# Optimization experiments

Measured on AMD Instinct MI355X. Metric: run time of the kernel, lower is better.

## Reference

```python
import jax, jax.numpy as jnp
import numpy as np

N_NODES = 50000
N_EDGES = 800000
N_GRAPHS = 128
IN_DIM, H1, H2, OUT_DIM = 256, 128, 64, 10


def setup_inputs() -> dict:
    key = jax.random.key(0)
    ks = jax.random.split(key, 8)
    x = jax.random.normal(ks[0], (N_NODES, IN_DIM), dtype=jnp.float32)
    edge_index = jax.random.randint(ks[1], (2, N_EDGES), 0, N_NODES, dtype=jnp.int64 if jax.config.jax_enable_x64 else jnp.int32)
    batch = jnp.sort(jax.random.randint(ks[2], (N_NODES,), 0, N_GRAPHS))
    s1 = 1.0 / np.sqrt(IN_DIM)
    s2 = 1.0 / np.sqrt(H1)
    s3 = 1.0 / np.sqrt(H2)
    W1 = jax.random.uniform(ks[3], (IN_DIM, H1), jnp.float32, -s1, s1)
    b1 = jnp.zeros((H1,), jnp.float32)
    W2 = jax.random.uniform(ks[4], (H1, H2), jnp.float32, -s2, s2)
    b2 = jnp.zeros((H2,), jnp.float32)
    Wfc = jax.random.uniform(ks[5], (H2, OUT_DIM), jnp.float32, -s3, s3)
    bfc = jax.random.uniform(ks[6], (OUT_DIM,), jnp.float32, -s3, s3)
    return {"x": x, "edge_index": edge_index, "batch": batch,
            "W1": W1, "b1": b1, "W2": W2, "b2": b2, "Wfc": Wfc, "bfc": bfc}


def _gcn_norm(edge_index, n_nodes):
    # PyG gcn_norm with add_self_loops=True: D^{-1/2} (A+I) D^{-1/2}
    self_loops = jnp.arange(n_nodes, dtype=edge_index.dtype)
    row = jnp.concatenate([edge_index[0], self_loops])
    col = jnp.concatenate([edge_index[1], self_loops])
    deg = jax.ops.segment_sum(jnp.ones_like(col, dtype=jnp.float32), col,
                              num_segments=n_nodes)
    dis = jnp.where(deg > 0, 1.0 / jnp.sqrt(deg), 0.0)
    norm = dis[row] * dis[col]  # [E + N]
    return row, col, norm


def _gcn_layer(x, W, b, row, col, norm, n_nodes):
    h = x @ W                          # [N, out]
    msg = h[row] * norm[:, None]       # gather + scale: [E+N, out]
    agg = jax.ops.segment_sum(msg, col, num_segments=n_nodes)
    return jax.nn.relu(agg + b)


def reference(x, edge_index, batch, W1, b1, W2, b2, Wfc, bfc):
    n = x.shape[0]
    row, col, norm = _gcn_norm(edge_index, n)
    h = _gcn_layer(x, W1, b1, row, col, norm, n)
    h = _gcn_layer(h, W2, b2, row, col, norm, n)
    # global max pool over graphs
    g = jax.ops.segment_max(h, batch, num_segments=N_GRAPHS)  # [G, H2]
    # dropout is identity at inference
    return g @ Wfc + bfc
```

## Files before the change

### kernel.cpp

```cpp
#include <hip/hip_runtime.h>
#include <math.h>


typedef __attribute__((ext_vector_type(8))) short bfrag;
typedef __attribute__((ext_vector_type(4))) float ffrag;

__device__ inline void bf16split(float f, short& hi, short& lo) {
    unsigned u = __float_as_uint(f);
    unsigned r = u + 0x7fffu + ((u >> 16) & 1u);
    unsigned short h = (unsigned short)(r >> 16);
    float hf = __uint_as_float(((unsigned)h) << 16);
    float lf = f - hf;
    unsigned ul = __float_as_uint(lf);
    unsigned rl = ul + 0x7fffu + ((ul >> 16) & 1u);
    hi = (short)h;
    lo = (short)(rl >> 16);
}

__global__ __launch_bounds__(256) void k_zero(int* __restrict__ cnt, int* __restrict__ pool,
                                              int n1, int n2) {
    int i = blockIdx.x * 256 + threadIdx.x;
    if (i < n1) cnt[i] = 0;
    if (i < n2) pool[i] = 0;
}

__global__ __launch_bounds__(256) void k_count(const int* __restrict__ ei, int* __restrict__ cnt,
                                               int E) {
    int e = blockIdx.x * 256 + threadIdx.x;
    if (e < E) atomicAdd(&cnt[ei[E + e]], 1);
}

__global__ __launch_bounds__(256) void k_dis(const int* __restrict__ cnt, float* __restrict__ dis,
                                             int N) {
    int v = blockIdx.x * 256 + threadIdx.x;
    if (v < N) dis[v] = 1.0f / sqrtf((float)(cnt[v] + 1));
}

__global__ __launch_bounds__(1024) void k_scan_block(const int* __restrict__ cnt,
                                                     int* __restrict__ rowptr,
                                                     int* __restrict__ bsum, int N) {
    __shared__ int lds[1024];
    int t = threadIdx.x;
    int i = blockIdx.x * 1024 + t;
    int val = (i < N) ? cnt[i] : 0;
    lds[t] = val;
    __syncthreads();
    for (int off = 1; off < 1024; off <<= 1) {
        int u = (t >= off) ? lds[t - off] : 0;
        __syncthreads();
        lds[t] += u;
        __syncthreads();
    }
    if (i < N) rowptr[i] = lds[t] - val;
    if (t == 1023) bsum[blockIdx.x] = lds[1023];
}

__global__ __launch_bounds__(1024) void k_scan_tot(const int* __restrict__ bsum,
                                                   int* __restrict__ bsum2, int nb) {
    __shared__ int lds[1024];
    int t = threadIdx.x;
    int val = (t < nb) ? bsum[t] : 0;
    lds[t] = val;
    __syncthreads();
    for (int off = 1; off < 1024; off <<= 1) {
        int u = (t >= off) ? lds[t - off] : 0;
        __syncthreads();
        lds[t] += u;
        __syncthreads();
    }
    if (t < nb) bsum2[t] = lds[t] - val;
}

__global__ __launch_bounds__(256) void k_scan_add(int* __restrict__ rowptr, int* __restrict__ cursor,
                                                  const int* __restrict__ bsum2, int N, int E) {
    int i = blockIdx.x * 256 + threadIdx.x;
    if (i < N) {
        int r = rowptr[i] + bsum2[i >> 10];
        rowptr[i] = r;
        cursor[i] = r;
    }
    if (i == 0) rowptr[N] = E;
}

__global__ __launch_bounds__(256) void k_fill(const int* __restrict__ ei,
                                              const float* __restrict__ dis,
                                              int* __restrict__ cursor,
                                              float2* __restrict__ csr, int E) {
    int e = blockIdx.x * 256 + threadIdx.x;
    if (e >= E) return;
    int r = ei[e];
    int c = ei[E + e];
    int p = atomicAdd(&cursor[c], 1);
    csr[p] = make_float2(__int_as_float(r), dis[r] * dis[c]);
}

__global__ __launch_bounds__(256) void k_wsplit(const float* __restrict__ W,
                                                short* __restrict__ wt_hi,
                                                short* __restrict__ wt_lo) {
    int i = blockIdx.x * 256 + threadIdx.x;
    if (i >= 256 * 128) return;
    int k = i >> 7, c = i & 127;
    short hi, lo;
    bf16split(W[i], hi, lo);
    wt_hi[c * 256 + k] = hi;
    wt_lo[c * 256 + k] = lo;
}

__global__ __launch_bounds__(256) void k_gemm1_mfma(const float* __restrict__ A,
                                                    const short* __restrict__ wt_hi,
                                                    const short* __restrict__ wt_lo,
                                                    float* __restrict__ C, int M) {
    constexpr int KD = 256;
    __shared__ short Ah[64][40];
    __shared__ short Al[64][40];

    const int t = threadIdx.x;
    const int lane = t & 63;
    const int wid = t >> 6;
    const int wr = wid >> 1;
    const int wc = wid & 1;
    const int row0 = blockIdx.x * 64;
    const int lrow = lane & 15;
    const int lkg = lane >> 4;

    ffrag acc[2][4];
#pragma unroll
    for (int mr = 0; mr < 2; mr++)
#pragma unroll
        for (int nr = 0; nr < 4; nr++)
#pragma unroll
            for (int q = 0; q < 4; q++) acc[mr][nr][q] = 0.f;

    for (int kc = 0; kc < KD; kc += 32) {
#pragma unroll
        for (int i = 0; i < 2; i++) {
            int s = t * 2 + i;
            int m = s >> 3;
            int kq = s & 7;
            int r = row0 + m;
            float4 v = make_float4(0.f, 0.f, 0.f, 0.f);
            if (r < M) v = *(const float4*)&A[(size_t)r * KD + kc + kq * 4];
            short4 sh, sl;
            bf16split(v.x, sh.x, sl.x);
            bf16split(v.y, sh.y, sl.y);
            bf16split(v.z, sh.z, sl.z);
            bf16split(v.w, sh.w, sl.w);
            *(short4*)&Ah[m][kq * 4] = sh;
            *(short4*)&Al[m][kq * 4] = sl;
        }
        __syncthreads();

        bfrag ahi[2], alo[2];
#pragma unroll
        for (int mr = 0; mr < 2; mr++) {
            int arow = wr * 32 + mr * 16 + lrow;
            ahi[mr] = *(const bfrag*)&Ah[arow][lkg * 8];
            alo[mr] = *(const bfrag*)&Al[arow][lkg * 8];
        }
#pragma unroll
        for (int nr = 0; nr < 4; nr++) {
            int col = wc * 64 + nr * 16 + lrow;
            const size_t boff = (size_t)col * 256 + kc + lkg * 8;
            bfrag bhi = *(const bfrag*)&wt_hi[boff];
            bfrag blo = *(const bfrag*)&wt_lo[boff];
#pragma unroll
            for (int mr = 0; mr < 2; mr++) {
                acc[mr][nr] = __builtin_amdgcn_mfma_f32_16x16x32_bf16(ahi[mr], bhi, acc[mr][nr], 0, 0, 0);
                acc[mr][nr] = __builtin_amdgcn_mfma_f32_16x16x32_bf16(ahi[mr], blo, acc[mr][nr], 0, 0, 0);
                acc[mr][nr] = __builtin_amdgcn_mfma_f32_16x16x32_bf16(alo[mr], bhi, acc[mr][nr], 0, 0, 0);
            }
        }
        __syncthreads();
    }

#pragma unroll
    for (int mr = 0; mr < 2; mr++)
#pragma unroll
        for (int nr = 0; nr < 4; nr++)
#pragma unroll
            for (int q = 0; q < 4; q++) {
                int rr = row0 + wr * 32 + mr * 16 + lkg * 4 + q;
                int cc = wc * 64 + nr * 16 + lrow;
                if (rr < M) C[(size_t)rr * 128 + cc] = acc[mr][nr][q];
            }
}

template <int KDIM, int NOUT>
__global__ __launch_bounds__(256) void k_gemm(const float* __restrict__ A,
                                              const float* __restrict__ W,
                                              float* __restrict__ C, int M) {
    constexpr int BM = 64, BK = 32;
    constexpr int NGRP = NOUT / 64;
    __shared__ float As[BK][BM + 4];
    __shared__ float Ws[BK][NOUT];

    const int t = threadIdx.x;
    const int tx = t & 15;
    const int ty = t >> 4;
    const int row0 = blockIdx.x * BM;

    float acc[4][4 * NGRP];
#pragma unroll
    for (int r = 0; r < 4; r++)
#pragma unroll
        for (int c = 0; c < 4 * NGRP; c++) acc[r][c] = 0.f;

    for (int kc = 0; kc < KDIM; kc += BK) {
#pragma unroll
        for (int i = 0; i < 2; i++) {
            int s = t * 2 + i;
            int m = s >> 3;
            int kq = s & 7;
            int r = row0 + m;
            float4 v = make_float4(0.f, 0.f, 0.f, 0.f);
            if (r < M) v = *(const float4*)&A[(size_t)r * KDIM + kc + kq * 4];
            As[kq * 4 + 0][m] = v.x;
            As[kq * 4 + 1][m] = v.y;
            As[kq * 4 + 2][m] = v.z;
            As[kq * 4 + 3][m] = v.w;
        }
        constexpr int WLOADS = (BK * NOUT / 4) / 256;
#pragma unroll
        for (int i = 0; i < WLOADS; i++) {
            int s = t + i * 256;
            int k = s / (NOUT / 4);
            int c4 = s % (NOUT / 4);
            *(float4*)&Ws[k][c4 * 4] = *(const float4*)&W[(size_t)(kc + k) * NOUT + c4 * 4];
        }
        __syncthreads();

#pragma unroll
        for (int k = 0; k < BK; k++) {
            float4 a = *(const float4*)&As[k][ty * 4];
            float4 w0 = *(const float4*)&Ws[k][tx * 4];
            float4 w1;
            if (NGRP == 2) w1 = *(const float4*)&Ws[k][64 + tx * 4];
            const float* ap = (const float*)&a;
            const float* w0p = (const float*)&w0;
            const float* w1p = (const float*)&w1;
#pragma unroll
            for (int r = 0; r < 4; r++) {
#pragma unroll
                for (int c = 0; c < 4; c++) {
                    acc[r][c] += ap[r] * w0p[c];
                    if (NGRP == 2) acc[r][4 + c] += ap[r] * w1p[c];
                }
            }
        }
        __syncthreads();
    }

#pragma unroll
    for (int r = 0; r < 4; r++) {
        int rr = row0 + ty * 4 + r;
        if (rr < M) {
            float4 o0 = make_float4(acc[r][0], acc[r][1], acc[r][2], acc[r][3]);
            *(float4*)&C[(size_t)rr * NOUT + tx * 4] = o0;
            if (NGRP == 2) {
                float4 o1 = make_float4(acc[r][4], acc[r][5], acc[r][6], acc[r][7]);
                *(float4*)&C[(size_t)rr * NOUT + 64 + tx * 4] = o1;
            }
        }
    }
}

__global__ __launch_bounds__(256) void k_agg1(const float* __restrict__ h,
                                              const int* __restrict__ rowptr,
                                              const float2* __restrict__ csr,
                                              const float* __restrict__ dis,
                                              const float* __restrict__ b,
                                              float* __restrict__ out, int N) {
    constexpr int U = 16;
    int wave = (blockIdx.x * 256 + threadIdx.x) >> 6;
    int lane = threadIdx.x & 63;
    if (wave >= N) return;
    const int v = wave;
    const float2* hp = (const float2*)h;
    float d = dis[v];
    float ds2 = d * d;
    float2 hv = hp[(size_t)v * 64 + lane];
    float ax = ds2 * hv.x, ay = ds2 * hv.y;
    int s0 = rowptr[v], s1 = rowptr[v + 1];

    if (s0 < s1) {
        int   uu[U];
        float ww[U];
#pragma unroll
        for (int q = 0; q < U; q++) {
            int jj = s0 + q;
            bool ok = jj < s1;
            float2 e = csr[ok ? jj : s0];
            uu[q] = ok ? __float_as_int(e.x) : 0;
            ww[q] = ok ? e.y : 0.f;
        }
        for (int j = s0; j < s1; j += U) {
            float2 g[U];
#pragma unroll
            for (int q = 0; q < U; q++) g[q] = hp[(size_t)uu[q] * 64 + lane];
            int   uu2[U];
            float ww2[U];
            int jn = j + U;
            if (jn < s1) {
#pragma unroll
                for (int q = 0; q < U; q++) {
                    int jj = jn + q;
                    bool ok = jj < s1;
                    float2 e = csr[ok ? jj : s0];
                    uu2[q] = ok ? __float_as_int(e.x) : 0;
                    ww2[q] = ok ? e.y : 0.f;
                }
            } else {
#pragma unroll
                for (int q = 0; q < U; q++) { uu2[q] = 0; ww2[q] = 0.f; }
            }
#pragma unroll
            for (int q = 0; q < U; q++) {
                ax += ww[q] * g[q].x;
                ay += ww[q] * g[q].y;
            }
#pragma unroll
            for (int q = 0; q < U; q++) { uu[q] = uu2[q]; ww[q] = ww2[q]; }
        }
    }
    float2 bb = *(const float2*)&b[lane * 2];
    float2 o;
    o.x = fmaxf(ax + bb.x, 0.f);
    o.y = fmaxf(ay + bb.y, 0.f);
    *(float2*)&out[(size_t)v * 128 + lane * 2] = o;
}

__global__ __launch_bounds__(256) void k_agg2_pool(const float* __restrict__ h,
                                                   const int* __restrict__ rowptr,
                                                   const float2* __restrict__ csr,
                                                   const float* __restrict__ dis,
                                                   const float* __restrict__ b,
                                                   const int* __restrict__ batch,
                                                   float* __restrict__ pool, int N) {
    constexpr int U = 16;
    int wave = (blockIdx.x * 256 + threadIdx.x) >> 6;
    int lane = threadIdx.x & 63;
    if (wave >= N) return;
    const int v = wave;
    float d = dis[v];
    float ds2 = d * d;
    float acc = ds2 * h[(size_t)v * 64 + lane];
    int s0 = rowptr[v], s1 = rowptr[v + 1];

    if (s0 < s1) {
        int   uu[U];
        float ww[U];
#pragma unroll
        for (int q = 0; q < U; q++) {
            int jj = s0 + q;
            bool ok = jj < s1;
            float2 e = csr[ok ? jj : s0];
            uu[q] = ok ? __float_as_int(e.x) : 0;
            ww[q] = ok ? e.y : 0.f;
        }
        for (int j = s0; j < s1; j += U) {
            float g[U];
#pragma unroll
            for (int q = 0; q < U; q++) g[q] = h[(size_t)uu[q] * 64 + lane];
            int   uu2[U];
            float ww2[U];
            int jn = j + U;
            if (jn < s1) {
#pragma unroll
                for (int q = 0; q < U; q++) {
                    int jj = jn + q;
                    bool ok = jj < s1;
                    float2 e = csr[ok ? jj : s0];
                    uu2[q] = ok ? __float_as_int(e.x) : 0;
                    ww2[q] = ok ? e.y : 0.f;
                }
            } else {
#pragma unroll
                for (int q = 0; q < U; q++) { uu2[q] = 0; ww2[q] = 0.f; }
            }
#pragma unroll
            for (int q = 0; q < U; q++) acc += ww[q] * g[q];
#pragma unroll
            for (int q = 0; q < U; q++) { uu[q] = uu2[q]; ww[q] = ww2[q]; }
        }
    }
    float val = fmaxf(acc + b[lane], 0.f);
    int g = batch[v];
    atomicMax((int*)&pool[(size_t)g * 64 + lane], __float_as_int(val));
}

__global__ __launch_bounds__(256) void k_fc(const float* __restrict__ pool,
                                            const float* __restrict__ Wfc,
                                            const float* __restrict__ bfc,
                                            float* __restrict__ out, int G) {
    int t = blockIdx.x * 256 + threadIdx.x;
    if (t >= G * 10) return;
    int g = t / 10, o = t % 10;
    float acc = bfc[o];
#pragma unroll
    for (int f = 0; f < 64; f++) acc += pool[g * 64 + f] * Wfc[f * 10 + o];
    out[t] = acc;
}

extern "C" void kernel_launch(void* const* d_in, const int* in_sizes, int n_in,
                              void* d_out, int out_size, void* d_ws, size_t ws_size,
                              hipStream_t stream) {
    const float* x   = (const float*)d_in[0];
    const int*   ei  = (const int*)d_in[1];
    const int*   bat = (const int*)d_in[2];
    const float* W1  = (const float*)d_in[3];
    const float* b1  = (const float*)d_in[4];
    const float* W2  = (const float*)d_in[5];
    const float* b2  = (const float*)d_in[6];
    const float* Wfc = (const float*)d_in[7];
    const float* bfc = (const float*)d_in[8];
    float* out = (float*)d_out;

    const int N = in_sizes[2];
    const int E = in_sizes[1] / 2;
    const int G = out_size / 10;

    char* ws = (char*)d_ws;
    size_t off = 0;
    auto alloc = [&](size_t bytes) -> char* {
        char* p = ws + off;
        off = (off + bytes + 255) & ~(size_t)255;
        return p;
    };
    int*    cnt    = (int*)alloc((size_t)N * 4);
    float*  dis    = (float*)alloc((size_t)N * 4);
    int*    rowptr = (int*)alloc((size_t)(N + 1) * 4);
    int*    cursor = (int*)alloc((size_t)N * 4);
    int*    bsum   = (int*)alloc(1024 * 4);
    int*    bsum2  = (int*)alloc(1024 * 4);
    float2* csr    = (float2*)alloc((size_t)E * 8);
    float*  h      = (float*)alloc((size_t)N * 128 * 4);
    float*  a1     = (float*)alloc((size_t)N * 128 * 4);
    float*  pool   = (float*)alloc((size_t)G * 64 * 4);
    short*  wt_hi  = (short*)alloc(128 * 256 * 2);
    short*  wt_lo  = (short*)alloc(128 * 256 * 2);
    (void)ws_size; (void)n_in;

    const int nb = (N + 1023) / 1024;

    {
        int zmax = N > G * 64 ? N : G * 64;
        k_zero<<<(zmax + 255) / 256, 256, 0, stream>>>(cnt, (int*)pool, N, G * 64);
    }
    k_wsplit<<<128, 256, 0, stream>>>(W1, wt_hi, wt_lo);
    k_count<<<(E + 255) / 256, 256, 0, stream>>>(ei, cnt, E);
    k_dis<<<(N + 255) / 256, 256, 0, stream>>>(cnt, dis, N);
    k_scan_block<<<nb, 1024, 0, stream>>>(cnt, rowptr, bsum, N);
    k_scan_tot<<<1, 1024, 0, stream>>>(bsum, bsum2, nb);
    k_scan_add<<<(N + 255) / 256, 256, 0, stream>>>(rowptr, cursor, bsum2, N, E);
    k_fill<<<(E + 255) / 256, 256, 0, stream>>>(ei, dis, cursor, csr, E);

    k_gemm1_mfma<<<(N + 63) / 64, 256, 0, stream>>>(x, wt_hi, wt_lo, h, N);
    k_agg1<<<(N * 64 + 255) / 256, 256, 0, stream>>>(h, rowptr, csr, dis, b1, a1, N);

    k_gemm<128, 64><<<(N + 63) / 64, 256, 0, stream>>>(a1, W2, h, N);
    k_agg2_pool<<<(N * 64 + 255) / 256, 256, 0, stream>>>(h, rowptr, csr, dis, b2, bat, pool, N);

    k_fc<<<(G * 10 + 255) / 256, 256, 0, stream>>>(pool, Wfc, bfc, out, G);
}
```

Baseline: 412.5 us.

## Split layer-1 aggregation across two waves per node and simplify gather loops

Layer-1 aggregation now assigns two wavefronts per node, each handling 64 of the 128 features as scalar floats, instead of one wave reading float2 per lane. Both aggregation kernels drop the software-pipelined 16-wide prefetch of CSR entries and use a plain 8-wide batch loop instead. The aim is more parallelism and fewer registers per wave, for better occupancy. In exchange the CSR index reads are duplicated across the two waves, each gather is narrower, and there is less memory-level parallelism per wave.

```diff
diff --git a/kernel.cpp b/kernel.cpp
--- a/kernel.cpp
+++ b/kernel.cpp
@@ -270,63 +270,33 @@
                                               const float* __restrict__ dis,
                                               const float* __restrict__ b,
                                               float* __restrict__ out, int N) {
-    constexpr int U = 16;
     int wave = (blockIdx.x * 256 + threadIdx.x) >> 6;
     int lane = threadIdx.x & 63;
-    if (wave >= N) return;
-    const int v = wave;
-    const float2* hp = (const float2*)h;
+    int v = wave >> 1;
+    int f = ((wave & 1) << 6) + lane;
+    if (v >= N) return;
     float d = dis[v];
     float ds2 = d * d;
-    float2 hv = hp[(size_t)v * 64 + lane];
-    float ax = ds2 * hv.x, ay = ds2 * hv.y;
+    float acc = ds2 * h[(size_t)v * 128 + f];
     int s0 = rowptr[v], s1 = rowptr[v + 1];
-
-    if (s0 < s1) {
-        int   uu[U];
-        float ww[U];
-#pragma unroll
-        for (int q = 0; q < U; q++) {
-            int jj = s0 + q;
+    for (int j = s0; j < s1; j += 8) {
+        int   uu[8];
+        float ww[8];
+#pragma unroll
+        for (int q = 0; q < 8; q++) {
+            int jj = j + q;
             bool ok = jj < s1;
             float2 e = csr[ok ? jj : s0];
             uu[q] = ok ? __float_as_int(e.x) : 0;
             ww[q] = ok ? e.y : 0.f;
         }
-        for (int j = s0; j < s1; j += U) {
-            float2 g[U];
-#pragma unroll
-            for (int q = 0; q < U; q++) g[q] = hp[(size_t)uu[q] * 64 + lane];
-            int   uu2[U];
-            float ww2[U];
-            int jn = j + U;
-            if (jn < s1) {
-#pragma unroll
-                for (int q = 0; q < U; q++) {
-                    int jj = jn + q;
-                    bool ok = jj < s1;
-                    float2 e = csr[ok ? jj : s0];
-                    uu2[q] = ok ? __float_as_int(e.x) : 0;
-                    ww2[q] = ok ? e.y : 0.f;
-                }
-            } else {
-#pragma unroll
-                for (int q = 0; q < U; q++) { uu2[q] = 0; ww2[q] = 0.f; }
-            }
-#pragma unroll
-            for (int q = 0; q < U; q++) {
-                ax += ww[q] * g[q].x;
-                ay += ww[q] * g[q].y;
-            }
-#pragma unroll
-            for (int q = 0; q < U; q++) { uu[q] = uu2[q]; ww[q] = ww2[q]; }
-        }
-    }
-    float2 bb = *(const float2*)&b[lane * 2];
-    float2 o;
-    o.x = fmaxf(ax + bb.x, 0.f);
-    o.y = fmaxf(ay + bb.y, 0.f);
-    *(float2*)&out[(size_t)v * 128 + lane * 2] = o;
+        float g[8];
+#pragma unroll
+        for (int q = 0; q < 8; q++) g[q] = h[(size_t)uu[q] * 128 + f];
+#pragma unroll
+        for (int q = 0; q < 8; q++) acc += ww[q] * g[q];
+    }
+    out[(size_t)v * 128 + f] = fmaxf(acc + b[f], 0.f);
 }
 
 __global__ __launch_bounds__(256) void k_agg2_pool(const float* __restrict__ h,
@@ -336,7 +306,6 @@
                                                    const float* __restrict__ b,
                                                    const int* __restrict__ batch,
                                                    float* __restrict__ pool, int N) {
-    constexpr int U = 16;
     int wave = (blockIdx.x * 256 + threadIdx.x) >> 6;
     int lane = threadIdx.x & 63;
     if (wave >= N) return;
@@ -345,43 +314,22 @@
     float ds2 = d * d;
     float acc = ds2 * h[(size_t)v * 64 + lane];
     int s0 = rowptr[v], s1 = rowptr[v + 1];
-
-    if (s0 < s1) {
-        int   uu[U];
-        float ww[U];
-#pragma unroll
-        for (int q = 0; q < U; q++) {
-            int jj = s0 + q;
+    for (int j = s0; j < s1; j += 8) {
+        int   uu[8];
+        float ww[8];
+#pragma unroll
+        for (int q = 0; q < 8; q++) {
+            int jj = j + q;
             bool ok = jj < s1;
             float2 e = csr[ok ? jj : s0];
             uu[q] = ok ? __float_as_int(e.x) : 0;
             ww[q] = ok ? e.y : 0.f;
         }
-        for (int j = s0; j < s1; j += U) {
-            float g[U];
-#pragma unroll
-            for (int q = 0; q < U; q++) g[q] = h[(size_t)uu[q] * 64 + lane];
-            int   uu2[U];
-            float ww2[U];
-            int jn = j + U;
-            if (jn < s1) {
-#pragma unroll
-                for (int q = 0; q < U; q++) {
-                    int jj = jn + q;
-                    bool ok = jj < s1;
-                    float2 e = csr[ok ? jj : s0];
-                    uu2[q] = ok ? __float_as_int(e.x) : 0;
-                    ww2[q] = ok ? e.y : 0.f;
-                }
-            } else {
-#pragma unroll
-                for (int q = 0; q < U; q++) { uu2[q] = 0; ww2[q] = 0.f; }
-            }
-#pragma unroll
-            for (int q = 0; q < U; q++) acc += ww[q] * g[q];
-#pragma unroll
-            for (int q = 0; q < U; q++) { uu[q] = uu2[q]; ww[q] = ww2[q]; }
-        }
+        float g[8];
+#pragma unroll
+        for (int q = 0; q < 8; q++) g[q] = h[(size_t)uu[q] * 64 + lane];
+#pragma unroll
+        for (int q = 0; q < 8; q++) acc += ww[q] * g[q];
     }
     float val = fmaxf(acc + b[lane], 0.f);
     int g = batch[v];
@@ -455,7 +403,10 @@
     k_fill<<<(E + 255) / 256, 256, 0, stream>>>(ei, dis, cursor, csr, E);
 
     k_gemm1_mfma<<<(N + 63) / 64, 256, 0, stream>>>(x, wt_hi, wt_lo, h, N);
-    k_agg1<<<(N * 64 + 255) / 256, 256, 0, stream>>>(h, rowptr, csr, dis, b1, a1, N);
+    {
+        long long waves = 2LL * N;
+        k_agg1<<<(int)((waves * 64 + 255) / 256), 256, 0, stream>>>(h, rowptr, csr, dis, b1, a1, N);
+    }
 
     k_gemm<128, 64><<<(N + 63) / 64, 256, 0, stream>>>(a1, W2, h, N);
     k_agg2_pool<<<(N * 64 + 255) / 256, 256, 0, stream>>>(h, rowptr, csr, dis, b2, bat, pool, N);
```

Result: no change. 416.4 us (+1.0%).
